# Optimization experiments

Measured on AMD Instinct MI355X. Metric: run time of the kernel, lower is better.

The kernel has to match this reference:

```python
import jax, jax.numpy as jnp
import numpy as np

N_QUBITS = 10
CNOT_CHAIN = [(i, i + 1) for i in range(N_QUBITS - 1)] + [(N_QUBITS - 1, 0)]


def setup_inputs() -> dict:
    key = jax.random.key(0)
    k1, k2, k3, k4 = jax.random.split(key, 4)
    B, S, E, F = 32, 512, 1024, 4096
    return {
        "x": jax.random.normal(k1, (B, S, N_QUBITS), dtype=jnp.float32),
        "q_params": jax.random.normal(k2, (N_QUBITS,), dtype=jnp.float32),
        "W1": jax.random.normal(k3, (F, N_QUBITS), dtype=jnp.float32) / np.sqrt(N_QUBITS),
        "W2": jax.random.normal(k4, (E, F), dtype=jnp.float32) / np.sqrt(F),
    }


def _simulate(angles):
    """Batched state-vector sim: RX(angle_i) on wire i from |0..0>, CNOT ring,
    then Pauli-Z expectation on every wire. angles: [N, n] -> [N, n]."""
    N, n = angles.shape
    half = 0.5 * angles
    c, s = jnp.cos(half), jnp.sin(half)
    # RX(theta)|0> = [cos(theta/2), -i sin(theta/2)]; per-qubit states [N, n, 2]
    qs = jnp.stack([c.astype(jnp.complex64), (-1j) * s.astype(jnp.complex64)], axis=-1)
    # product state via iterated Kronecker product -> [N, 2^n]
    state = qs[:, 0]
    for i in range(1, n):
        state = (state[:, :, None] * qs[:, i][:, None, :]).reshape(N, -1)
    state = state.reshape((N,) + (2,) * n)  # axis i+1 <-> wire i
    # CNOT(src, tgt): flip target amplitudes on the control=1 half (permutation)
    for src, tgt in CNOT_CHAIN:
        s0, s1 = jnp.split(state, 2, axis=src + 1)
        state = jnp.concatenate([s0, jnp.flip(s1, axis=tgt + 1)], axis=src + 1)
    probs = (state.real ** 2 + state.imag ** 2).reshape(N, -1)  # [N, 2^n]
    # <Z_i> = sum_k p_k * (1 - 2*bit_i(k)); wire 0 is the most-significant bit
    bits = (jnp.arange(2 ** n)[:, None] >> (n - 1 - jnp.arange(n))) & 1
    signs = (1 - 2 * bits).astype(probs.dtype)  # [2^n, n]
    return probs @ signs


def reference(x, q_params, W1, W2):
    B, S, n = x.shape
    # back-to-back RX on the same wire commute: angles add
    angles = (x + q_params).reshape(B * S, n)
    q_out = _simulate(angles).reshape(B, S, n)
    # dropout is identity at inference; it sits before ReLU and is a no-op here
    h = jax.nn.relu(q_out @ W1.T)  # [B, S, ffn_dim]
    return h @ W2.T  # [B, S, embed_dim]
```

## Files before the change

kernel.cpp:

```cpp
#include <hip/hip_runtime.h>
#include <hip/hip_bf16.h>

typedef __bf16 bf16x8 __attribute__((ext_vector_type(8)));
typedef float f32x16 __attribute__((ext_vector_type(16)));

#define NQ     10
#define M_ROWS 16384
#define N_COLS 1024
#define K_DIM  4096

__device__ __forceinline__ void gload_lds16(const __hip_bfloat16* g, __hip_bfloat16* l) {
  __builtin_amdgcn_global_load_lds(
      (const __attribute__((address_space(1))) void*)g,
      (__attribute__((address_space(3))) void*)l,
      16, 0, 0);
}

__global__ void __launch_bounds__(256) prep(const float* __restrict__ W1,
                                            const float* __restrict__ W2,
                                            const float* __restrict__ x,
                                            const float* __restrict__ qp,
                                            __hip_bfloat16* __restrict__ W2b,
                                            __hip_bfloat16* __restrict__ Wq,
                                            __hip_bfloat16* __restrict__ Qb) {
  const int b = blockIdx.x;
  const int tid = threadIdx.x;
  if (b < 4096) {
    int i = (b * 256 + tid) * 4;
    float4 v = *(const float4*)(W2 + i);
    union { __hip_bfloat16 h[4]; uint2 u; } p;
    p.h[0] = __float2bfloat16(v.x);
    p.h[1] = __float2bfloat16(v.y);
    p.h[2] = __float2bfloat16(v.z);
    p.h[3] = __float2bfloat16(v.w);
    *(uint2*)(W2b + i) = p.u;
  } else if (b < 4112) {
    int kcol = (b - 4096) * 256 + tid;
    union { __hip_bfloat16 h[16]; uint4 u[2]; } p;
#pragma unroll
    for (int j = 0; j < NQ; j++) p.h[j] = __float2bfloat16(W1[kcol * NQ + j]);
#pragma unroll
    for (int j = NQ; j < 16; j++) p.h[j] = __float2bfloat16(0.f);
    *(uint4*)(Wq + kcol * 16) = p.u[0];
    *(uint4*)(Wq + kcol * 16 + 8) = p.u[1];
  } else {
    int row = (b - 4112) * 256 + tid;
    float c[NQ];
#pragma unroll
    for (int j = 0; j < NQ; j++) c[j] = cosf(x[row * NQ + j] + qp[j]);
    float q[NQ];
    float prod19 = 1.f;
#pragma unroll
    for (int j = 1; j < NQ; j++) prod19 *= c[j];
    q[0] = prod19;
    float pref = c[0];
#pragma unroll
    for (int k = 1; k < NQ; k++) { pref *= c[k]; q[k] = pref; }
    union { __hip_bfloat16 h[16]; uint4 u[2]; } p;
#pragma unroll
    for (int j = 0; j < NQ; j++) p.h[j] = __float2bfloat16(q[j]);
#pragma unroll
    for (int j = NQ; j < 16; j++) p.h[j] = __float2bfloat16(0.f);
    *(uint4*)(Qb + row * 16) = p.u[0];
    *(uint4*)(Qb + row * 16 + 8) = p.u[1];
  }
}

__global__ void __launch_bounds__(512, 2) gemm_fused(const __hip_bfloat16* __restrict__ Qb,
                                                     const __hip_bfloat16* __restrict__ Wq,
                                                     const __hip_bfloat16* __restrict__ B,
                                                     float* __restrict__ C) {
  __shared__ __align__(16) __hip_bfloat16 As[2][256 * 64];
  __shared__ __align__(16) __hip_bfloat16 Bs[2][256 * 64];

  const int tid  = threadIdx.x;
  const int wave = tid >> 6;
  const int lane = tid & 63;
  const int l31  = lane & 31;
  const int l5   = lane >> 5;
  const int l7   = l31 & 7;
  const int wm   = (wave >> 2) * 128;
  const int wn   = (wave & 3) * 64;

  const int L    = blockIdx.x;
  const int xcd  = L & 7;
  const int idx  = L >> 3;
  const int col0 = (xcd >> 1) * 256;
  const int row0 = (((xcd & 1) << 5) + idx) * 256;

  const int ldrow = lane >> 3;
  const int ldc   = (((lane & 7) ^ ldrow) << 3);

  const bf16x8 qb = *(const bf16x8*)(Qb + (row0 + wave * 32 + l31) * 16 + l5 * 8);

  f32x16 acc[4][2];
#pragma unroll
  for (int i = 0; i < 4; i++)
#pragma unroll
    for (int j = 0; j < 2; j++)
#pragma unroll
      for (int r = 0; r < 16; r++) acc[i][j][r] = 0.f;

#define WQF(t, kt) (*(const bf16x8*)(Wq + ((t) * 64 + (kt) * 32 + l31) * 16 + l5 * 8))

#define STAGE(bw, ts, i)                                                              \
  gload_lds16(B + (col0 + wave * 32 + (i) * 8 + ldrow) * K_DIM + (ts) * 64 + ldc,     \
              &Bs[bw][(wave * 32 + (i) * 8) * 64])

#define MINI(bw, wqf, kt) do {                                                        \
    f32x16 d_;                                                                        \
    _Pragma("unroll") for (int r_ = 0; r_ < 16; r_++) d_[r_] = 0.f;                   \
    d_ = __builtin_amdgcn_mfma_f32_32x32x16_bf16((wqf), qb, d_, 0, 0, 0);             \
    const int hb_ = (wave * 32 + l31) * 64;                                           \
    _Pragma("unroll") for (int q_ = 0; q_ < 4; q_++) {                                \
      union { __hip_bfloat16 h[4]; ushort4 u; } p_;                                   \
      _Pragma("unroll") for (int r_ = 0; r_ < 4; r_++)                                \
        p_.h[r_] = __float2bfloat16(fmaxf(d_[4 * q_ + r_], 0.f));                     \
      *(ushort4*)(&As[bw][hb_ + ((((kt) * 4 + q_) ^ l7) << 3) + 4 * l5]) = p_.u;      \
    }                                                                                 \
  } while (0)

#define MFMA_BF16 __builtin_amdgcn_mfma_f32_32x32x16_bf16
#define NOTAIL
#define TAILW asm volatile("s_waitcnt vmcnt(2)" ::)

#define PHASE(br, kki, TAIL) do {                                                     \
    const int ch_ = (((2 * (kki) + l5) ^ l7) << 3);                                   \
    const bf16x8 af0 = *(const bf16x8*)(&As[br][(wm +  0 + l31) * 64 + ch_]);         \
    const bf16x8 af1 = *(const bf16x8*)(&As[br][(wm + 32 + l31) * 64 + ch_]);         \
    const bf16x8 af2 = *(const bf16x8*)(&As[br][(wm + 64 + l31) * 64 + ch_]);         \
    const bf16x8 af3 = *(const bf16x8*)(&As[br][(wm + 96 + l31) * 64 + ch_]);         \
    const bf16x8 bb0 = *(const bf16x8*)(&Bs[br][(wn +  0 + l31) * 64 + ch_]);         \
    const bf16x8 bb1 = *(const bf16x8*)(&Bs[br][(wn + 32 + l31) * 64 + ch_]);         \
    __builtin_amdgcn_s_barrier();                                                     \
    asm volatile("s_waitcnt lgkmcnt(0)" ::);                                          \
    __builtin_amdgcn_sched_barrier(0);                                                \
    __builtin_amdgcn_s_setprio(1);                                                    \
    acc[0][0] = MFMA_BF16(af0, bb0, acc[0][0], 0, 0, 0);                              \
    acc[1][0] = MFMA_BF16(af1, bb0, acc[1][0], 0, 0, 0);                              \
    acc[2][0] = MFMA_BF16(af2, bb0, acc[2][0], 0, 0, 0);                              \
    acc[3][0] = MFMA_BF16(af3, bb0, acc[3][0], 0, 0, 0);                              \
    acc[0][1] = MFMA_BF16(af0, bb1, acc[0][1], 0, 0, 0);                              \
    acc[1][1] = MFMA_BF16(af1, bb1, acc[1][1], 0, 0, 0);                              \
    acc[2][1] = MFMA_BF16(af2, bb1, acc[2][1], 0, 0, 0);                              \
    acc[3][1] = MFMA_BF16(af3, bb1, acc[3][1], 0, 0, 0);                              \
    __builtin_amdgcn_s_setprio(0);                                                    \
    TAIL;                                                                             \
    __builtin_amdgcn_s_barrier();                                                     \
  } while (0)

#define TILE(br, bw, wqu0, wqu1, wqp0, wqp1, t) do {                                  \
    STAGE(bw, (t) + 1, 0); STAGE(bw, (t) + 1, 1);                                     \
    MINI(bw, wqu0, 0);                                                                \
    PHASE(br, 0, NOTAIL);                                                             \
    STAGE(bw, (t) + 1, 2); STAGE(bw, (t) + 1, 3);                                     \
    MINI(bw, wqu1, 1);                                                                \
    PHASE(br, 1, NOTAIL);                                                             \
    PHASE(br, 2, NOTAIL);                                                             \
    wqp0 = WQF((t) + 2, 0); wqp1 = WQF((t) + 2, 1);                                   \
    PHASE(br, 3, TAILW);                                                              \
  } while (0)

  STAGE(0, 0, 0); STAGE(0, 0, 1); STAGE(0, 0, 2); STAGE(0, 0, 3);
  bf16x8 wqA0 = WQF(0, 0), wqA1 = WQF(0, 1);
  bf16x8 wqB0 = WQF(1, 0), wqB1 = WQF(1, 1);
  MINI(0, wqA0, 0);
  MINI(0, wqA1, 1);
  __syncthreads();

  for (int u = 0; u < 32; u++) {
    TILE(0, 1, wqB0, wqB1, wqA0, wqA1, 2 * u);
    TILE(1, 0, wqA0, wqA1, wqB0, wqB1, 2 * u + 1);
  }

#pragma unroll
  for (int fm = 0; fm < 4; fm++) {
#pragma unroll
    for (int fn = 0; fn < 2; fn++) {
      const int colb = col0 + wn + fn * 32 + l31;
      const int rowb = row0 + wm + fm * 32 + 4 * l5;
#pragma unroll
      for (int reg = 0; reg < 16; reg++) {
        int row = rowb + (reg & 3) + 8 * (reg >> 2);
        C[row * N_COLS + colb] = acc[fm][fn][reg];
      }
    }
  }
}

extern "C" void kernel_launch(void* const* d_in, const int* in_sizes, int n_in,
                              void* d_out, int out_size, void* d_ws, size_t ws_size,
                              hipStream_t stream) {
  const float* x  = (const float*)d_in[0];
  const float* qp = (const float*)d_in[1];
  const float* W1 = (const float*)d_in[2];
  const float* W2 = (const float*)d_in[3];
  float* out = (float*)d_out;

  char* ws = (char*)d_ws;
  __hip_bfloat16* W2b = (__hip_bfloat16*)ws;
  __hip_bfloat16* Wq  = (__hip_bfloat16*)(ws + 8388608);
  __hip_bfloat16* Qb  = (__hip_bfloat16*)(ws + 8519680);

  prep<<<4176, 256, 0, stream>>>(W1, W2, x, qp, W2b, Wq, Qb);
  gemm_fused<<<256, 512, 0, stream>>>(Qb, Wq, W2b, out);
}
```

Baseline: 250.1 us.

## Double-buffer LDS fragment registers to prefetch next k-phase during MFMAs

Splits each phase into a separate fragment load and MFMA core, using two register sets (X/Y) so the LDS reads for the next k-step are issued before the current step's MFMAs. The wait before the MFMAs is relaxed to lgkmcnt(6) so the prefetched loads can stay in flight. The MINI computations and the Wq/B staging are reordered, and the tail wait becomes vmcnt(0) so the next buffer's fragments can be loaded at the end of the tile. This aims to hide LDS latency behind matrix math, at the cost of more VGPRs and a fragile dependence on the waitcnt counts being correct.

```diff
diff --git a/kernel.cpp b/kernel.cpp
--- a/kernel.cpp
+++ b/kernel.cpp
@@ -101,6 +101,9 @@
 #pragma unroll
       for (int r = 0; r < 16; r++) acc[i][j][r] = 0.f;
 
+  bf16x8 Xa0, Xa1, Xa2, Xa3, Xb0, Xb1;
+  bf16x8 Ya0, Ya1, Ya2, Ya3, Yb0, Yb1;
+
 #define WQF(t, kt) (*(const bf16x8*)(Wq + ((t) * 64 + (kt) * 32 + l31) * 16 + l5 * 8))
 
 #define STAGE(bw, ts, i)                                                              \
@@ -120,45 +123,52 @@
     }                                                                                 \
   } while (0)
 
+#define LOADF(SET, buf, kki) do {                                                     \
+    const int ch_ = (((2 * (kki) + l5) ^ l7) << 3);                                   \
+    SET##a0 = *(const bf16x8*)(&As[buf][(wm +  0 + l31) * 64 + ch_]);                 \
+    SET##a1 = *(const bf16x8*)(&As[buf][(wm + 32 + l31) * 64 + ch_]);                 \
+    SET##a2 = *(const bf16x8*)(&As[buf][(wm + 64 + l31) * 64 + ch_]);                 \
+    SET##a3 = *(const bf16x8*)(&As[buf][(wm + 96 + l31) * 64 + ch_]);                 \
+    SET##b0 = *(const bf16x8*)(&Bs[buf][(wn +  0 + l31) * 64 + ch_]);                 \
+    SET##b1 = *(const bf16x8*)(&Bs[buf][(wn + 32 + l31) * 64 + ch_]);                 \
+  } while (0)
+
 #define MFMA_BF16 __builtin_amdgcn_mfma_f32_32x32x16_bf16
 #define NOTAIL
-#define TAILW asm volatile("s_waitcnt vmcnt(2)" ::)
-
-#define PHASE(br, kki, TAIL) do {                                                     \
-    const int ch_ = (((2 * (kki) + l5) ^ l7) << 3);                                   \
-    const bf16x8 af0 = *(const bf16x8*)(&As[br][(wm +  0 + l31) * 64 + ch_]);         \
-    const bf16x8 af1 = *(const bf16x8*)(&As[br][(wm + 32 + l31) * 64 + ch_]);         \
-    const bf16x8 af2 = *(const bf16x8*)(&As[br][(wm + 64 + l31) * 64 + ch_]);         \
-    const bf16x8 af3 = *(const bf16x8*)(&As[br][(wm + 96 + l31) * 64 + ch_]);         \
-    const bf16x8 bb0 = *(const bf16x8*)(&Bs[br][(wn +  0 + l31) * 64 + ch_]);         \
-    const bf16x8 bb1 = *(const bf16x8*)(&Bs[br][(wn + 32 + l31) * 64 + ch_]);         \
+#define TAILW asm volatile("s_waitcnt vmcnt(0)" ::)
+
+#define PHASE_CORE(SET, TAIL) do {                                                    \
     __builtin_amdgcn_s_barrier();                                                     \
-    asm volatile("s_waitcnt lgkmcnt(0)" ::);                                          \
+    asm volatile("s_waitcnt lgkmcnt(6)" ::);                                          \
     __builtin_amdgcn_sched_barrier(0);                                                \
     __builtin_amdgcn_s_setprio(1);                                                    \
-    acc[0][0] = MFMA_BF16(af0, bb0, acc[0][0], 0, 0, 0);                              \
-    acc[1][0] = MFMA_BF16(af1, bb0, acc[1][0], 0, 0, 0);                              \
-    acc[2][0] = MFMA_BF16(af2, bb0, acc[2][0], 0, 0, 0);                              \
-    acc[3][0] = MFMA_BF16(af3, bb0, acc[3][0], 0, 0, 0);                              \
-    acc[0][1] = MFMA_BF16(af0, bb1, acc[0][1], 0, 0, 0);                              \
-    acc[1][1] = MFMA_BF16(af1, bb1, acc[1][1], 0, 0, 0);                              \
-    acc[2][1] = MFMA_BF16(af2, bb1, acc[2][1], 0, 0, 0);                              \
-    acc[3][1] = MFMA_BF16(af3, bb1, acc[3][1], 0, 0, 0);                              \
+    acc[0][0] = MFMA_BF16(SET##a0, SET##b0, acc[0][0], 0, 0, 0);                      \
+    acc[1][0] = MFMA_BF16(SET##a1, SET##b0, acc[1][0], 0, 0, 0);                      \
+    acc[2][0] = MFMA_BF16(SET##a2, SET##b0, acc[2][0], 0, 0, 0);                      \
+    acc[3][0] = MFMA_BF16(SET##a3, SET##b0, acc[3][0], 0, 0, 0);                      \
+    acc[0][1] = MFMA_BF16(SET##a0, SET##b1, acc[0][1], 0, 0, 0);                      \
+    acc[1][1] = MFMA_BF16(SET##a1, SET##b1, acc[1][1], 0, 0, 0);                      \
+    acc[2][1] = MFMA_BF16(SET##a2, SET##b1, acc[2][1], 0, 0, 0);                      \
+    acc[3][1] = MFMA_BF16(SET##a3, SET##b1, acc[3][1], 0, 0, 0);                      \
     __builtin_amdgcn_s_setprio(0);                                                    \
     TAIL;                                                                             \
     __builtin_amdgcn_s_barrier();                                                     \
   } while (0)
 
 #define TILE(br, bw, wqu0, wqu1, wqp0, wqp1, t) do {                                  \
+    MINI(bw, wqu0, 0);                                                                \
     STAGE(bw, (t) + 1, 0); STAGE(bw, (t) + 1, 1);                                     \
-    MINI(bw, wqu0, 0);                                                                \
-    PHASE(br, 0, NOTAIL);                                                             \
+    LOADF(Y, br, 1);                                                                  \
+    PHASE_CORE(X, NOTAIL);                                                            \
+    MINI(bw, wqu1, 1);                                                                \
+    wqp0 = WQF((t) + 2, 0); wqp1 = WQF((t) + 2, 1);                                   \
     STAGE(bw, (t) + 1, 2); STAGE(bw, (t) + 1, 3);                                     \
-    MINI(bw, wqu1, 1);                                                                \
-    PHASE(br, 1, NOTAIL);                                                             \
-    PHASE(br, 2, NOTAIL);                                                             \
-    wqp0 = WQF((t) + 2, 0); wqp1 = WQF((t) + 2, 1);                                   \
-    PHASE(br, 3, TAILW);                                                              \
+    LOADF(X, br, 2);                                                                  \
+    PHASE_CORE(Y, NOTAIL);                                                            \
+    LOADF(Y, br, 3);                                                                  \
+    PHASE_CORE(X, TAILW);                                                             \
+    LOADF(X, bw, 0);                                                                  \
+    PHASE_CORE(Y, NOTAIL);                                                            \
   } while (0)
 
   STAGE(0, 0, 0); STAGE(0, 0, 1); STAGE(0, 0, 2); STAGE(0, 0, 3);
@@ -167,6 +177,7 @@
   MINI(0, wqA0, 0);
   MINI(0, wqA1, 1);
   __syncthreads();
+  LOADF(X, 0, 0);
 
   for (int u = 0; u < 32; u++) {
     TILE(0, 1, wqB0, wqB1, wqA0, wqA1, 2 * u);
```

Result: no change. 245.5 us (-1.8%).
